# Optimization experiments

Hardware: AMD Instinct MI355X
Metric: run time of the kernel (lower is better)

## Reference

```python
import jax, jax.numpy as jnp
import numpy as np

MATRY_DIMS = (64, 128, 256, 512, 768)   # nested matryoshka prefix dims
TEMPERATURE = 0.05                      # SimCSE default
REL_IMPORTANCE = np.ones(len(MATRY_DIMS), dtype=np.float32)
EPS = 1e-8                              # torch cosine_similarity eps


def _contrastive_loss_one_dim(emb1, emb2, d):
    # prefix-slice to matryoshka dim d, cosine-sim matrix, softmax CE vs arange labels
    a = emb1[:, :d]
    b = emb2[:, :d]
    a = a / jnp.maximum(jnp.linalg.norm(a, axis=-1, keepdims=True), EPS)
    b = b / jnp.maximum(jnp.linalg.norm(b, axis=-1, keepdims=True), EPS)
    logits = jnp.einsum('id,jd->ij', a, b) / TEMPERATURE  # [N, N]
    logp = jax.nn.log_softmax(logits, axis=-1)
    # CrossEntropyLoss with labels = arange(N): mean of -logp[i, i]
    return -jnp.mean(jnp.diagonal(logp))


def setup_inputs() -> dict:
    key = jax.random.key(0)
    k1, k2 = jax.random.split(key)
    N, D = 8192, 768
    return {
        'emb1': jax.random.normal(k1, (N, D), dtype=jnp.float32),
        'emb2': jax.random.normal(k2, (N, D), dtype=jnp.float32),
    }


def reference(emb1, emb2):
    losses = jnp.stack([_contrastive_loss_one_dim(emb1, emb2, d) for d in MATRY_DIMS])
    weighted = jnp.asarray(REL_IMPORTANCE) * losses
    return jnp.sum(weighted)
```

## Files before the change

kernel.cpp:

```cpp
#include <hip/hip_runtime.h>
#include <math.h>

typedef __attribute__((ext_vector_type(4))) float f32x4;
typedef __attribute__((ext_vector_type(4))) int   i32x4;
typedef __attribute__((ext_vector_type(8))) int   i32x8;

#define N_ROWS 8192
#define DFULL 768
#define KSC (1.4426950408889634f / 0.05f)
#define NEGSH (-28.853900817779268f)
#define LN2 0.6931471805599453f
#define PLB32 ((size_t)N_ROWS * 32)

__global__ __launch_bounds__(192) void mcl_prep(
    const float* __restrict__ e1, const float* __restrict__ e2,
    char* __restrict__ h1, char* __restrict__ h2,
    float* __restrict__ inv1, float* __restrict__ inv2)
{
  const int b = blockIdx.x;
  const int mat = b >> 13, row = b & (N_ROWS - 1);
  const float* src = (mat ? e2 : e1) + (size_t)row * DFULL;
  char* dst = mat ? h2 : h1;
  float* invo = mat ? inv2 : inv1;
  const int t = threadIdx.x;
  const int k = t * 4;

  const f32x4 v = *(const f32x4*)(src + k);
  const float s = v[0]*v[0] + v[1]*v[1] + v[2]*v[2] + v[3]*v[3];
  float p0 = (k < 64)  ? s : 0.f;
  float p1 = (k < 128) ? s : 0.f;
  float p2 = (k < 256) ? s : 0.f;
  float p3 = (k < 512) ? s : 0.f;
  float p4 = s;

  const int lo = __builtin_amdgcn_cvt_pk_fp8_f32(v[0], v[1], 0, false);
  const int pk = __builtin_amdgcn_cvt_pk_fp8_f32(v[2], v[3], lo, true);
  *(int*)(dst + (size_t)(k >> 5) * PLB32 + (size_t)row * 32 + (k & 31)) = pk;

#pragma unroll
  for (int off = 32; off > 0; off >>= 1) {
    p0 += __shfl_down(p0, off, 64);
    p1 += __shfl_down(p1, off, 64);
    p2 += __shfl_down(p2, off, 64);
    p3 += __shfl_down(p3, off, 64);
    p4 += __shfl_down(p4, off, 64);
  }
  __shared__ float red[3][5];
  const int lane = t & 63, w = t >> 6;
  if (lane == 0) { red[w][0]=p0; red[w][1]=p1; red[w][2]=p2; red[w][3]=p3; red[w][4]=p4; }
  __syncthreads();
  if (t == 0) {
#pragma unroll
    for (int q = 0; q < 5; ++q) {
      const float sum = red[0][q] + red[1][q] + red[2][q];
      invo[q * N_ROWS + row] = 1.f / fmaxf(sqrtf(sum), 1e-8f);
    }
  }
}

__global__ __launch_bounds__(256, 2) void mcl_main(
    const char* __restrict__ h1, const char* __restrict__ h2,
    const float* __restrict__ inv1, const float* __restrict__ inv2,
    float* __restrict__ diag, float* __restrict__ partial)
{
  __shared__ float rowsumW[2][5][128];

  const int tid = threadIdx.x;
  const int lane = tid & 63, wid = tid >> 6;
  const int wr = wid >> 1, wc = wid & 1;
  const int l15 = lane & 15, lh = lane >> 4;

  const int id = blockIdx.x;
  const int nid = (id & 7) * 512 + (id >> 3);
  const int st = nid >> 6, tt = nid & 63;
  const int bi = ((st >> 3) << 3) + (tt >> 3);
  const int bj = ((st & 7) << 3) + (tt & 7);
  const int rowA0 = bi * 128, rowB0 = bj * 128;

  const char* pa = h1 + (size_t)lh * PLB32 + (size_t)(rowA0 + wr * 64 + l15) * 32;
  const char* pb = h2 + (size_t)lh * PLB32 + (size_t)(rowB0 + wc * 64 + l15) * 32;

  f32x4 acc[4][4];
#pragma unroll
  for (int n = 0; n < 4; ++n)
#pragma unroll
    for (int m = 0; m < 4; ++m) acc[n][m] = (f32x4)0.f;

#define LOADF(DST, P) do {                                                     \
    const i32x4 lo_ = *(const i32x4*)(P);                                      \
    const i32x4 hi_ = *(const i32x4*)((P) + 16);                               \
    DST = __builtin_shufflevector(lo_, hi_, 0, 1, 2, 3, 4, 5, 6, 7); } while (0)

#define SUMEXP(RP, U) do {                                                     \
    RP += __builtin_amdgcn_exp2f((U)[0]) + __builtin_amdgcn_exp2f((U)[1]) +    \
          __builtin_amdgcn_exp2f((U)[2]) + __builtin_amdgcn_exp2f((U)[3]); } while (0)

#define REDUCE_STORE(RP, DCP) do {                                             \
    _Pragma("unroll")                                                          \
    for (int m = 0; m < 4; ++m) {                                              \
      float v_ = (RP)[m];                                                      \
      v_ += __shfl_xor(v_, 16, 64);                                            \
      v_ += __shfl_xor(v_, 32, 64);                                            \
      if (lh == 0) rowsumW[wc][(DCP)][wr * 64 + m * 16 + l15] = v_;            \
    } } while (0)

#define EPI(DCP) do {                                                          \
    float s1K[4];                                                              \
    _Pragma("unroll")                                                          \
    for (int m = 0; m < 4; ++m)                                                \
      s1K[m] = inv1[(DCP) * N_ROWS + rowA0 + wr * 64 + m * 16 + l15] * KSC;    \
    float rp[4] = {0.f, 0.f, 0.f, 0.f};                                        \
    _Pragma("unroll")                                                          \
    for (int n = 0; n < 4; ++n) {                                              \
      const f32x4 s2 = *(const f32x4*)(inv2 + (DCP) * N_ROWS + rowB0 +         \
                                       wc * 64 + n * 16 + (lh << 2));          \
      _Pragma("unroll")                                                        \
      for (int m = 0; m < 4; ++m) {                                            \
        const f32x4 u = acc[n][m] * s2 * s1K[m] + NEGSH;                       \
        SUMEXP(rp[m], u);                                                      \
      }                                                                        \
    }                                                                          \
    REDUCE_STORE(rp, (DCP));                                                   \
    if (bi == bj && wr == wc && lh == (l15 >> 2)) {                            \
      const int rgd = l15 & 3;                                                 \
      _Pragma("unroll")                                                        \
      for (int m = 0; m < 4; ++m) {                                            \
        const float s2d = inv2[(DCP) * N_ROWS + rowB0 + wc * 64 + m * 16 + l15];\
        diag[(DCP) * N_ROWS + rowA0 + wr * 64 + m * 16 + l15] =                \
            acc[m][m][rgd] * s1K[m] * s2d * LN2;                               \
      }                                                                        \
    } } while (0)

  {
    i32x8 af[4], bf[4];
#pragma unroll
    for (int m = 0; m < 4; ++m) { LOADF(af[m], pa + m * 512); }
#pragma unroll
    for (int n = 0; n < 4; ++n) { LOADF(bf[n], pb + n * 512); }
    const int msk = (lh < 2) ? 0x7F : 0x00;
    float s1K0[4], s1K1[4];
#pragma unroll
    for (int m = 0; m < 4; ++m) {
      s1K0[m] = inv1[0 * N_ROWS + rowA0 + wr * 64 + m * 16 + l15] * KSC;
      s1K1[m] = inv1[1 * N_ROWS + rowA0 + wr * 64 + m * 16 + l15] * KSC;
    }
    float rp0[4] = {0.f, 0.f, 0.f, 0.f};
    float rp1[4] = {0.f, 0.f, 0.f, 0.f};
#pragma unroll
    for (int n = 0; n < 4; ++n) {
      const f32x4 s20 = *(const f32x4*)(inv2 + 0 * N_ROWS + rowB0 + wc * 64 + n * 16 + (lh << 2));
      const f32x4 s21 = *(const f32x4*)(inv2 + 1 * N_ROWS + rowB0 + wc * 64 + n * 16 + (lh << 2));
#pragma unroll
      for (int m = 0; m < 4; ++m) {
        const f32x4 t = __builtin_amdgcn_mfma_scale_f32_16x16x128_f8f6f4(
            bf[n], af[m], (f32x4)0.f, 0, 0, 0, msk, 0, msk);
        acc[n][m] = __builtin_amdgcn_mfma_scale_f32_16x16x128_f8f6f4(
            bf[n], af[m], acc[n][m], 0, 0, 0, 0x7F, 0, 0x7F);
        const f32x4 u0 = t * s20 * s1K0[m] + NEGSH;
        SUMEXP(rp0[m], u0);
        const f32x4 u1 = acc[n][m] * s21 * s1K1[m] + NEGSH;
        SUMEXP(rp1[m], u1);
        if (n == m && bi == bj && wr == wc && lh == (l15 >> 2)) {
          const int rgd = l15 & 3;
          const float s2d0 = inv2[0 * N_ROWS + rowB0 + wc * 64 + m * 16 + l15];
          const float s2d1 = inv2[1 * N_ROWS + rowB0 + wc * 64 + m * 16 + l15];
          diag[0 * N_ROWS + rowA0 + wr * 64 + m * 16 + l15] = t[rgd] * s1K0[m] * s2d0 * LN2;
          diag[1 * N_ROWS + rowA0 + wr * 64 + m * 16 + l15] = acc[m][m][rgd] * s1K1[m] * s2d1 * LN2;
        }
      }
    }
    REDUCE_STORE(rp0, 0);
    REDUCE_STORE(rp1, 1);
    pa += 4 * PLB32;
    pb += 4 * PLB32;
  }

#pragma unroll 1
  for (int ck = 1; ck < 6; ++ck) {
    i32x8 af[4], bf[4];
#pragma unroll
    for (int m = 0; m < 4; ++m) { LOADF(af[m], pa + m * 512); }
#pragma unroll
    for (int n = 0; n < 4; ++n) { LOADF(bf[n], pb + n * 512); }
    __builtin_amdgcn_s_setprio(1);
#pragma unroll
    for (int n = 0; n < 4; ++n)
#pragma unroll
      for (int m = 0; m < 4; ++m)
        acc[n][m] = __builtin_amdgcn_mfma_scale_f32_16x16x128_f8f6f4(
            bf[n], af[m], acc[n][m], 0, 0, 0, 0x7F, 0, 0x7F);
    __builtin_amdgcn_s_setprio(0);
    if (ck == 1)      EPI(2);
    else if (ck == 3) EPI(3);
    else if (ck == 5) EPI(4);
    pa += 4 * PLB32;
    pb += 4 * PLB32;
  }
#undef EPI
#undef REDUCE_STORE
#undef SUMEXP
#undef LOADF

  __syncthreads();
  for (int x = tid; x < 5 * 128; x += 256) {
    const int d = x >> 7, r = x & 127;
    partial[((size_t)bj * 5 + d) * N_ROWS + rowA0 + r] =
        rowsumW[0][d][r] + rowsumW[1][d][r];
  }
}

__global__ __launch_bounds__(256) void mcl_reduce(
    const float* __restrict__ partial, const float* __restrict__ diag,
    float* __restrict__ out)
{
  const int item = blockIdx.x * 256 + threadIdx.x;
  const int d = item >> 13;
  const int i = item & (N_ROWS - 1);
  float s = 0.f;
#pragma unroll 4
  for (int bj = 0; bj < 64; ++bj)
    s += partial[((size_t)bj * 5 + d) * N_ROWS + i];
  float term = (20.0f + logf(s) - diag[d * N_ROWS + i]) * (1.0f / 8192.0f);
#pragma unroll
  for (int off = 32; off > 0; off >>= 1) term += __shfl_down(term, off, 64);
  __shared__ float red[4];
  const int lane = threadIdx.x & 63, w = threadIdx.x >> 6;
  if (lane == 0) red[w] = term;
  __syncthreads();
  if (threadIdx.x == 0) atomicAdd(out, red[0] + red[1] + red[2] + red[3]);
}

extern "C" void kernel_launch(void* const* d_in, const int* in_sizes, int n_in,
                              void* d_out, int out_size, void* d_ws, size_t ws_size,
                              hipStream_t stream) {
  const float* e1 = (const float*)d_in[0];
  const float* e2 = (const float*)d_in[1];
  char* ws = (char*)d_ws;

  const size_t HBYTES = (size_t)N_ROWS * DFULL;
  const size_t IBYTES = (size_t)5 * N_ROWS * sizeof(float);
  char*  h1      = ws;
  char*  h2      = ws + HBYTES;
  float* inv1    = (float*)(ws + 2 * HBYTES);
  float* inv2    = (float*)(ws + 2 * HBYTES + IBYTES);
  float* diag    = (float*)(ws + 2 * HBYTES + 2 * IBYTES);
  float* partial = (float*)(ws + 2 * HBYTES + 3 * IBYTES);
  const size_t NEED = 2 * HBYTES + 3 * IBYTES + (size_t)64 * 5 * N_ROWS * sizeof(float);
  if (ws_size < NEED) return;

  hipMemsetAsync(d_out, 0, sizeof(float) * out_size, stream);
  mcl_prep<<<2 * N_ROWS, 192, 0, stream>>>(e1, e2, h1, h2, inv1, inv2);
  mcl_main<<<4096, 256, 0, stream>>>(h1, h2, inv1, inv2, diag, partial);
  mcl_reduce<<<160, 256, 0, stream>>>(partial, diag, (float*)d_out);
}
```

Baseline: 133.8 us.

## Fully unroll chunk loop and overlap next-chunk loads with exp epilogues

Replaces the runtime chunk loop with a fully unrolled sequence. Each epilogue's exp-sum now runs after the next chunk's fragment loads are issued and before that chunk's MFMAs, so memory latency can hide behind the transcendental work. The scale vectors are also prefetched ahead of time, and the diagonal reuses the loaded inv2 vector instead of doing a separate load. The risk is higher register pressure from holding the loaded fragments live across the epilogue, at a 2-waves-per-SIMD launch bound.

```diff
diff --git a/kernel.cpp b/kernel.cpp
--- a/kernel.cpp
+++ b/kernel.cpp
@@ -69,6 +69,7 @@
   const int lane = tid & 63, wid = tid >> 6;
   const int wr = wid >> 1, wc = wid & 1;
   const int l15 = lane & 15, lh = lane >> 4;
+  const int rgd = l15 & 3;
 
   const int id = blockIdx.x;
   const int nid = (id & 7) * 512 + (id >> 3);
@@ -76,6 +77,7 @@
   const int bi = ((st >> 3) << 3) + (tt >> 3);
   const int bj = ((st & 7) << 3) + (tt & 7);
   const int rowA0 = bi * 128, rowB0 = bj * 128;
+  const bool dgb = (bi == bj) && (wr == wc) && (lh == (l15 >> 2));
 
   const char* pa = h1 + (size_t)lh * PLB32 + (size_t)(rowA0 + wr * 64 + l15) * 32;
   const char* pb = h2 + (size_t)lh * PLB32 + (size_t)(rowB0 + wc * 64 + l15) * 32;
@@ -86,10 +88,27 @@
 #pragma unroll
     for (int m = 0; m < 4; ++m) acc[n][m] = (f32x4)0.f;
 
-#define LOADF(DST, P) do {                                                     \
-    const i32x4 lo_ = *(const i32x4*)(P);                                      \
-    const i32x4 hi_ = *(const i32x4*)((P) + 16);                               \
-    DST = __builtin_shufflevector(lo_, hi_, 0, 1, 2, 3, 4, 5, 6, 7); } while (0)
+#define LOADF(CK) do {                                                         \
+    _Pragma("unroll")                                                          \
+    for (int m = 0; m < 4; ++m) {                                              \
+      const i32x4 alo = *(const i32x4*)(pa + (CK) * 4 * PLB32 + m * 512);      \
+      const i32x4 ahi = *(const i32x4*)(pa + (CK) * 4 * PLB32 + m * 512 + 16); \
+      af[m] = __builtin_shufflevector(alo, ahi, 0, 1, 2, 3, 4, 5, 6, 7);       \
+      const i32x4 blo = *(const i32x4*)(pb + (CK) * 4 * PLB32 + m * 512);      \
+      const i32x4 bhi = *(const i32x4*)(pb + (CK) * 4 * PLB32 + m * 512 + 16); \
+      bf[m] = __builtin_shufflevector(blo, bhi, 0, 1, 2, 3, 4, 5, 6, 7);       \
+    } } while (0)
+
+#define MFMACL(CK) do {                                                        \
+    __builtin_amdgcn_s_setprio(1);                                             \
+    _Pragma("unroll")                                                          \
+    for (int n = 0; n < 4; ++n)                                                \
+      _Pragma("unroll")                                                        \
+      for (int m = 0; m < 4; ++m)                                              \
+        acc[n][m] = __builtin_amdgcn_mfma_scale_f32_16x16x128_f8f6f4(          \
+            bf[n], af[m], acc[n][m], 0, 0, 0, 0x7F, 0, 0x7F);                  \
+    __builtin_amdgcn_s_setprio(0);                                             \
+  } while (0)
 
 #define SUMEXP(RP, U) do {                                                     \
     RP += __builtin_amdgcn_exp2f((U)[0]) + __builtin_amdgcn_exp2f((U)[1]) +    \
@@ -104,101 +123,102 @@
       if (lh == 0) rowsumW[wc][(DCP)][wr * 64 + m * 16 + l15] = v_;            \
     } } while (0)
 
-#define EPI(DCP) do {                                                          \
-    float s1K[4];                                                              \
+#define EPIPRE(DCP, S1, S2) do {                                               \
     _Pragma("unroll")                                                          \
     for (int m = 0; m < 4; ++m)                                                \
-      s1K[m] = inv1[(DCP) * N_ROWS + rowA0 + wr * 64 + m * 16 + l15] * KSC;    \
+      S1[m] = inv1[(DCP) * N_ROWS + rowA0 + wr * 64 + m * 16 + l15] * KSC;     \
+    _Pragma("unroll")                                                          \
+    for (int n = 0; n < 4; ++n)                                                \
+      S2[n] = *(const f32x4*)(inv2 + (DCP) * N_ROWS + rowB0 + wc * 64 +        \
+                              n * 16 + (lh << 2));                             \
+  } while (0)
+
+#define EPIMAIN(DCP, S1, S2) do {                                              \
     float rp[4] = {0.f, 0.f, 0.f, 0.f};                                        \
     _Pragma("unroll")                                                          \
-    for (int n = 0; n < 4; ++n) {                                              \
-      const f32x4 s2 = *(const f32x4*)(inv2 + (DCP) * N_ROWS + rowB0 +         \
-                                       wc * 64 + n * 16 + (lh << 2));          \
+    for (int n = 0; n < 4; ++n)                                                \
       _Pragma("unroll")                                                        \
       for (int m = 0; m < 4; ++m) {                                            \
-        const f32x4 u = acc[n][m] * s2 * s1K[m] + NEGSH;                       \
+        const f32x4 u = acc[n][m] * S2[n] * S1[m] + NEGSH;                     \
         SUMEXP(rp[m], u);                                                      \
       }                                                                        \
-    }                                                                          \
     REDUCE_STORE(rp, (DCP));                                                   \
-    if (bi == bj && wr == wc && lh == (l15 >> 2)) {                            \
-      const int rgd = l15 & 3;                                                 \
+    if (dgb) {                                                                 \
       _Pragma("unroll")                                                        \
-      for (int m = 0; m < 4; ++m) {                                            \
-        const float s2d = inv2[(DCP) * N_ROWS + rowB0 + wc * 64 + m * 16 + l15];\
+      for (int m = 0; m < 4; ++m)                                              \
         diag[(DCP) * N_ROWS + rowA0 + wr * 64 + m * 16 + l15] =                \
-            acc[m][m][rgd] * s1K[m] * s2d * LN2;                               \
-      }                                                                        \
+            acc[m][m][rgd] * S1[m] * S2[m][rgd] * LN2;                         \
     } } while (0)
 
-  {
-    i32x8 af[4], bf[4];
-#pragma unroll
-    for (int m = 0; m < 4; ++m) { LOADF(af[m], pa + m * 512); }
-#pragma unroll
-    for (int n = 0; n < 4; ++n) { LOADF(bf[n], pb + n * 512); }
+  i32x8 af[4], bf[4];
+
+  {
+    float s1a[4]; f32x4 s2a[4];
+    EPIPRE(0, s1a, s2a);
+    LOADF(0);
     const int msk = (lh < 2) ? 0x7F : 0x00;
-    float s1K0[4], s1K1[4];
-#pragma unroll
-    for (int m = 0; m < 4; ++m) {
-      s1K0[m] = inv1[0 * N_ROWS + rowA0 + wr * 64 + m * 16 + l15] * KSC;
-      s1K1[m] = inv1[1 * N_ROWS + rowA0 + wr * 64 + m * 16 + l15] * KSC;
-    }
     float rp0[4] = {0.f, 0.f, 0.f, 0.f};
-    float rp1[4] = {0.f, 0.f, 0.f, 0.f};
 #pragma unroll
     for (int n = 0; n < 4; ++n) {
-      const f32x4 s20 = *(const f32x4*)(inv2 + 0 * N_ROWS + rowB0 + wc * 64 + n * 16 + (lh << 2));
-      const f32x4 s21 = *(const f32x4*)(inv2 + 1 * N_ROWS + rowB0 + wc * 64 + n * 16 + (lh << 2));
-#pragma unroll
-      for (int m = 0; m < 4; ++m) {
-        const f32x4 t = __builtin_amdgcn_mfma_scale_f32_16x16x128_f8f6f4(
+      f32x4 t[4];
+#pragma unroll
+      for (int m = 0; m < 4; ++m)
+        t[m] = __builtin_amdgcn_mfma_scale_f32_16x16x128_f8f6f4(
             bf[n], af[m], (f32x4)0.f, 0, 0, 0, msk, 0, msk);
-        acc[n][m] = __builtin_amdgcn_mfma_scale_f32_16x16x128_f8f6f4(
-            bf[n], af[m], acc[n][m], 0, 0, 0, 0x7F, 0, 0x7F);
-        const f32x4 u0 = t * s20 * s1K0[m] + NEGSH;
-        SUMEXP(rp0[m], u0);
-        const f32x4 u1 = acc[n][m] * s21 * s1K1[m] + NEGSH;
-        SUMEXP(rp1[m], u1);
-        if (n == m && bi == bj && wr == wc && lh == (l15 >> 2)) {
-          const int rgd = l15 & 3;
-          const float s2d0 = inv2[0 * N_ROWS + rowB0 + wc * 64 + m * 16 + l15];
-          const float s2d1 = inv2[1 * N_ROWS + rowB0 + wc * 64 + m * 16 + l15];
-          diag[0 * N_ROWS + rowA0 + wr * 64 + m * 16 + l15] = t[rgd] * s1K0[m] * s2d0 * LN2;
-          diag[1 * N_ROWS + rowA0 + wr * 64 + m * 16 + l15] = acc[m][m][rgd] * s1K1[m] * s2d1 * LN2;
-        }
-      }
-    }
-    REDUCE_STORE(rp0, 0);
-    REDUCE_STORE(rp1, 1);
-    pa += 4 * PLB32;
-    pb += 4 * PLB32;
-  }
-
-#pragma unroll 1
-  for (int ck = 1; ck < 6; ++ck) {
-    i32x8 af[4], bf[4];
-#pragma unroll
-    for (int m = 0; m < 4; ++m) { LOADF(af[m], pa + m * 512); }
-#pragma unroll
-    for (int n = 0; n < 4; ++n) { LOADF(bf[n], pb + n * 512); }
-    __builtin_amdgcn_s_setprio(1);
-#pragma unroll
-    for (int n = 0; n < 4; ++n)
 #pragma unroll
       for (int m = 0; m < 4; ++m)
         acc[n][m] = __builtin_amdgcn_mfma_scale_f32_16x16x128_f8f6f4(
             bf[n], af[m], acc[n][m], 0, 0, 0, 0x7F, 0, 0x7F);
-    __builtin_amdgcn_s_setprio(0);
-    if (ck == 1)      EPI(2);
-    else if (ck == 3) EPI(3);
-    else if (ck == 5) EPI(4);
-    pa += 4 * PLB32;
-    pb += 4 * PLB32;
-  }
-#undef EPI
+#pragma unroll
+      for (int m = 0; m < 4; ++m) {
+        const f32x4 u0 = t[m] * s2a[n] * s1a[m] + NEGSH;
+        SUMEXP(rp0[m], u0);
+      }
+      if (dgb)
+        diag[0 * N_ROWS + rowA0 + wr * 64 + n * 16 + l15] =
+            t[n][rgd] * s1a[n] * s2a[n][rgd] * LN2;
+    }
+    REDUCE_STORE(rp0, 0);
+  }
+
+  {
+    float s1b[4]; f32x4 s2b[4];
+    EPIPRE(1, s1b, s2b);
+    LOADF(1);
+    EPIMAIN(1, s1b, s2b);
+    MFMACL(1);
+  }
+  {
+    float s1c[4]; f32x4 s2c[4];
+    EPIPRE(2, s1c, s2c);
+    LOADF(2);
+    EPIMAIN(2, s1c, s2c);
+    MFMACL(2);
+  }
+  {
+    LOADF(3);
+    MFMACL(3);
+  }
+  {
+    float s1d[4]; f32x4 s2d4[4];
+    EPIPRE(3, s1d, s2d4);
+    LOADF(4);
+    EPIMAIN(3, s1d, s2d4);
+    MFMACL(4);
+  }
+  {
+    float s1e[4]; f32x4 s2e[4];
+    EPIPRE(4, s1e, s2e);
+    LOADF(5);
+    MFMACL(5);
+    EPIMAIN(4, s1e, s2e);
+  }
+
+#undef EPIMAIN
+#undef EPIPRE
 #undef REDUCE_STORE
 #undef SUMEXP
+#undef MFMACL
 #undef LOADF
 
   __syncthreads();
```

Measured after the change: 128.3 us. -4.1%, faster.
